# Performance work log

Measured on AMD Instinct MI355X. Metric: run time of the kernel, lower is better.

The kernel has to match this reference:

```python
import jax, jax.numpy as jnp
import numpy as np

T, N, F = 8, 4096, 128
LPF, HPF, H, LP_HID, E = 128, 128, 256, 256, 131072
D = LPF + HPF


def setup_inputs() -> dict:
    key = jax.random.key(0)
    ks = jax.random.split(key, 16)
    s = lambda k, *shape: jax.random.normal(k, shape, dtype=jnp.float32) * 0.05
    feats = jax.random.normal(ks[0], (T, N, F), dtype=jnp.float32)
    # row-stochastic-ish propagation matrices
    p = jax.random.uniform(ks[1], (T, N, N), dtype=jnp.float32)
    p = p / jnp.sum(p, axis=-1, keepdims=True)
    eidx = jax.random.randint(ks[2], (2, E), 0, N, dtype=jnp.int64)
    return {
        "features": feats,
        "p_matrix": p,
        "predict_edge_index": eidx,
        "W_lpf": s(ks[3], F, LPF), "b_lpf": jnp.zeros((LPF,), jnp.float32),
        "W_hpf": s(ks[4], F, HPF), "b_hpf": jnp.zeros((HPF,), jnp.float32),
        "W_ih": s(ks[5], 4 * H, D), "W_hh": s(ks[6], 4 * H, H),
        "b_ih": jnp.zeros((4 * H,), jnp.float32), "b_hh": jnp.zeros((4 * H,), jnp.float32),
        "W1": s(ks[7], 2 * H, LP_HID), "b1": jnp.zeros((LP_HID,), jnp.float32),
        "W2": s(ks[8], LP_HID, 1), "b2": jnp.zeros((1,), jnp.float32),
    }


def reference(features, p_matrix, predict_edge_index, W_lpf, b_lpf, W_hpf, b_hpf,
              W_ih, W_hh, b_ih, b_hh, W1, b1, W2, b2):
    # --- batched low/high-pass graph filters over all T snapshots ---
    xw = jnp.einsum('tnf,fd->tnd', features, W_lpf)          # X @ W_lp
    low = jax.nn.relu(jnp.einsum('tnm,tmd->tnd', p_matrix, xw) + b_lpf)
    px = jnp.einsum('tnm,tmf->tnf', p_matrix, features)      # P @ X
    high = jax.nn.relu(jnp.einsum('tnf,fd->tnd', features - px, W_hpf) + b_hpf)
    x_seq = jnp.concatenate([low, high], axis=-1)            # [T, N, D]

    # --- LSTM over time, nodes as batch (torch gate order i,f,g,o) ---
    def step(carry, x_t):
        h, c = carry
        gates = x_t @ W_ih.T + h @ W_hh.T + (b_ih + b_hh)    # [N, 4H]
        i, f, g, o = jnp.split(gates, 4, axis=-1)
        c = jax.nn.sigmoid(f) * c + jax.nn.sigmoid(i) * jnp.tanh(g)
        h = jax.nn.sigmoid(o) * jnp.tanh(c)
        return (h, c), None

    h0 = jnp.zeros((N, H), x_seq.dtype)
    (h_fin, _), _ = jax.lax.scan(step, (h0, h0), x_seq)      # final timestep hidden

    # --- gather + concat + MLP link predictor ---
    src = h_fin[predict_edge_index[0]]
    dst = h_fin[predict_edge_index[1]]
    comb = jnp.concatenate([src, dst], axis=-1)              # [E, 2H]
    hid = jax.nn.relu(comb @ W1 + b1)
    logits = (hid @ W2 + b2).squeeze(-1)                     # [E]
    return logits
```

## Files before the change

kernel.cpp:

```cpp
#include <hip/hip_runtime.h>
#include <stdint.h>

#define T_ 8
#define N_ 4096
#define E_ 131072

typedef __attribute__((ext_vector_type(4))) float f32x4;
typedef __attribute__((ext_vector_type(8))) short s16x8;
typedef __attribute__((ext_vector_type(4))) short s16x4;

static __device__ __forceinline__ short f2bf(float f) {
    union { float f; unsigned u; } v; v.f = f;
    unsigned r = v.u + 0x7fffu + ((v.u >> 16) & 1u);
    return (short)(r >> 16);
}
static __device__ __forceinline__ float bf2f(short s) {
    union { float f; unsigned u; } v; v.u = ((unsigned)(unsigned short)s) << 16;
    return v.f;
}

static __device__ __forceinline__ void bar_nodrain() {
    asm volatile("s_waitcnt lgkmcnt(0)\n\ts_barrier" ::: "memory");
}

__global__ __launch_bounds__(256) void pack_yt(const float* __restrict__ feat,
                                               short* __restrict__ yt) {
    __shared__ float tile[32][33];
    const int t = blockIdx.z, j0 = blockIdx.y * 32, n0 = blockIdx.x * 32;
    const float* src = feat + (size_t)t * N_ * 128 + j0;
    const int jj = threadIdx.x & 31, i4 = threadIdx.x >> 5;
#pragma unroll
    for (int s = 0; s < 4; s++) {
        int ii = i4 * 4 + s;
        tile[ii][jj] = src[(size_t)(n0 + ii) * 128 + jj];
    }
    __syncthreads();
    const int nn = threadIdx.x & 31, j4 = threadIdx.x >> 5;
#pragma unroll
    for (int s = 0; s < 4; s++) {
        int j2 = j4 * 4 + s;
        yt[(size_t)(t * 128 + j0 + j2) * N_ + n0 + nn] = f2bf(tile[nn][j2]);
    }
}

__global__ __launch_bounds__(512) void pfy_gemm(const float* __restrict__ P,
                                                const short* __restrict__ Yt,
                                                float* __restrict__ Z) {
    __shared__ short As[2][128][72];
    __shared__ short Bs[2][128][72];
    const int t = blockIdx.y;
    const int m0 = blockIdx.x * 128;
    const int tid = threadIdx.x;
    const int lane = tid & 63, wid = tid >> 6;
    const int wm = wid >> 2, wn = wid & 3;
    const int frow = lane & 15, kq = lane >> 4;

    const float* Pt = P + (size_t)t * N_ * N_;
    const short* Bt = Yt + (size_t)t * 128 * N_;

    const int ar = tid >> 2;
    const int ak16 = (tid & 3) * 16;
    const int bj = tid >> 2;
    const int bk16 = (tid & 3) * 16;

    f32x4 acc[4][2];
    f32x4 zf = {0.f, 0.f, 0.f, 0.f};
#pragma unroll
    for (int m = 0; m < 4; m++)
#pragma unroll
        for (int n = 0; n < 2; n++) acc[m][n] = zf;

    f32x4 aA[4], aB[4]; s16x8 bA[2], bB[2];

    const float* Pr = &Pt[(size_t)(m0 + ar) * 4096 + ak16];
    const short* Br = &Bt[(size_t)bj * 4096 + bk16];

#define LOADA(KT) do { const int k0_ = (KT) * 64;                              \
        _Pragma("unroll") for (int i = 0; i < 4; i++)                          \
            aA[i] = *(const f32x4*)&Pr[k0_ + i * 4];                           \
        _Pragma("unroll") for (int i = 0; i < 2; i++)                          \
            bA[i] = *(const s16x8*)&Br[k0_ + i * 8]; } while (0)
#define LOADB(KT) do { const int k0_ = (KT) * 64;                              \
        _Pragma("unroll") for (int i = 0; i < 4; i++)                          \
            aB[i] = *(const f32x4*)&Pr[k0_ + i * 4];                           \
        _Pragma("unroll") for (int i = 0; i < 2; i++)                          \
            bB[i] = *(const s16x8*)&Br[k0_ + i * 8]; } while (0)
#define STOREA(BUF) do {                                                       \
        _Pragma("unroll") for (int i = 0; i < 4; i++) {                        \
            s16x4 c4_;                                                         \
            _Pragma("unroll") for (int j = 0; j < 4; j++) c4_[j] = f2bf(aA[i][j]); \
            *(s16x4*)&As[BUF][ar][ak16 + i * 4] = c4_; }                       \
        _Pragma("unroll") for (int i = 0; i < 2; i++)                          \
            *(s16x8*)&Bs[BUF][bj][bk16 + i * 8] = bA[i]; } while (0)
#define STOREB(BUF) do {                                                       \
        _Pragma("unroll") for (int i = 0; i < 4; i++) {                        \
            s16x4 c4_;                                                         \
            _Pragma("unroll") for (int j = 0; j < 4; j++) c4_[j] = f2bf(aB[i][j]); \
            *(s16x4*)&As[BUF][ar][ak16 + i * 4] = c4_; }                       \
        _Pragma("unroll") for (int i = 0; i < 2; i++)                          \
            *(s16x8*)&Bs[BUF][bj][bk16 + i * 8] = bB[i]; } while (0)

    auto compute_t = [&](int buf) {
#pragma unroll
        for (int ks = 0; ks < 2; ks++) {
            s16x8 af[4], bfr[2];
#pragma unroll
            for (int m = 0; m < 4; m++)
                af[m] = *(const s16x8*)&As[buf][wm * 64 + m * 16 + frow][kq * 8 + ks * 32];
#pragma unroll
            for (int n = 0; n < 2; n++)
                bfr[n] = *(const s16x8*)&Bs[buf][wn * 32 + n * 16 + frow][kq * 8 + ks * 32];
#pragma unroll
            for (int m = 0; m < 4; m++)
#pragma unroll
                for (int n = 0; n < 2; n++)
                    acc[m][n] = __builtin_amdgcn_mfma_f32_16x16x32_bf16(af[m], bfr[n], acc[m][n], 0, 0, 0);
        }
    };

    LOADA(0);
    STOREA(0);
    LOADB(1);
    LOADA(2);
    bar_nodrain();

#pragma unroll 2
    for (int kt = 0; kt < 64; kt++) {
        compute_t(kt & 1);
        if (kt < 63) {
            if ((kt & 1) == 0) {
                STOREB(1);
                if (kt + 3 < 64) LOADB(kt + 3);
            } else {
                STOREA(0);
                if (kt + 3 < 64) LOADA(kt + 3);
            }
            bar_nodrain();
        }
    }
#undef LOADA
#undef LOADB
#undef STOREA
#undef STOREB

    float* Zt = Z + (size_t)t * N_ * 128;
#pragma unroll
    for (int m = 0; m < 4; m++)
#pragma unroll
        for (int n = 0; n < 2; n++)
#pragma unroll
            for (int r = 0; r < 4; r++) {
                int row = m0 + wm * 64 + m * 16 + kq * 4 + r;
                int col = wn * 32 + n * 16 + frow;
                Zt[(size_t)row * 128 + col] = acc[m][n][r];
            }
}

__global__ __launch_bounds__(256) void hp2_gemm(const float* __restrict__ feat,
                                                const float* __restrict__ PX,
                                                const float* __restrict__ Wlp,
                                                const float* __restrict__ Whp,
                                                const float* __restrict__ b_lpf,
                                                const float* __restrict__ b_hpf,
                                                short* __restrict__ xhi,
                                                short* __restrict__ xlo) {
    __shared__ float As[32][68];
    __shared__ float Ws[32][132];
    const int m0 = blockIdx.x * 64;
    const int mode = blockIdx.y;
    const float* W = mode ? Whp : Wlp;
    const float* bp = mode ? b_hpf : b_lpf;
    const int tid = threadIdx.x;
    const int rg = tid & 15, cg2 = tid >> 4;
    float acc[4][8];
#pragma unroll
    for (int r = 0; r < 4; r++)
#pragma unroll
        for (int c = 0; c < 8; c++) acc[r][c] = 0.f;

    for (int k0 = 0; k0 < 128; k0 += 32) {
#pragma unroll
        for (int s = 0; s < 2; s++) {
            int q = tid + s * 256, row = q >> 3, k4 = q & 7;
            f32x4 pv = *(const f32x4*)&PX[(size_t)(m0 + row) * 128 + k0 + k4 * 4];
            f32x4 v;
            if (mode) {
                f32x4 fv = *(const f32x4*)&feat[(size_t)(m0 + row) * 128 + k0 + k4 * 4];
#pragma unroll
                for (int i = 0; i < 4; i++) v[i] = fv[i] - pv[i];
            } else {
                v = pv;
            }
#pragma unroll
            for (int i = 0; i < 4; i++) As[k4 * 4 + i][row] = v[i];
        }
#pragma unroll
        for (int s = 0; s < 4; s++) {
            int q = tid + s * 256, kk = q >> 5, j4 = q & 31;
            *(f32x4*)&Ws[kk][j4 * 4] = *(const f32x4*)&W[(size_t)(k0 + kk) * 128 + j4 * 4];
        }
        __syncthreads();
#pragma unroll
        for (int kk = 0; kk < 32; kk++) {
            f32x4 a  = *(const f32x4*)&As[kk][rg * 4];
            f32x4 w0 = *(const f32x4*)&Ws[kk][cg2 * 8];
            f32x4 w1 = *(const f32x4*)&Ws[kk][cg2 * 8 + 4];
#pragma unroll
            for (int r = 0; r < 4; r++)
#pragma unroll
                for (int c = 0; c < 4; c++) {
                    acc[r][c]     += a[r] * w0[c];
                    acc[r][c + 4] += a[r] * w1[c];
                }
        }
        __syncthreads();
    }
    float bh[8];
#pragma unroll
    for (int c = 0; c < 8; c++) bh[c] = bp[cg2 * 8 + c];
#pragma unroll
    for (int r = 0; r < 4; r++) {
        s16x4 h0, h1, l0, l1;
#pragma unroll
        for (int c = 0; c < 4; c++) {
            float v0 = fmaxf(acc[r][c] + bh[c], 0.f);
            float v1 = fmaxf(acc[r][c + 4] + bh[c + 4], 0.f);
            h0[c] = f2bf(v0); l0[c] = f2bf(v0 - bf2f(h0[c]));
            h1[c] = f2bf(v1); l1[c] = f2bf(v1 - bf2f(h1[c]));
        }
        size_t base = (size_t)(m0 + rg * 4 + r) * 256 + mode * 128 + cg2 * 8;
        *(s16x4*)&xhi[base] = h0;  *(s16x4*)&xhi[base + 4] = h1;
        *(s16x4*)&xlo[base] = l0;  *(s16x4*)&xlo[base + 4] = l1;
    }
}

__global__ __launch_bounds__(256) void pack_all(const float* __restrict__ W1,
                                                const float* __restrict__ W_ih,
                                                const float* __restrict__ W_hh,
                                                const float* __restrict__ b_ih,
                                                const float* __restrict__ b_hh,
                                                short* __restrict__ w1chi,
                                                short* __restrict__ w1clo,
                                                short* __restrict__ wchi,
                                                short* __restrict__ wclo,
                                                float* __restrict__ bsum) {
    __shared__ float tile[32][33];
    const int b = blockIdx.x;
    if (b < 512) {
        int idx = (b * 256 + threadIdx.x) * 4;
        int j = idx >> 9, k = idx & 511;
        int orig = (j & 3) * 256 + (j >> 2);
        const float* src = (k < 256) ? &W_ih[(size_t)orig * 256 + k]
                                     : &W_hh[(size_t)orig * 256 + (k - 256)];
        f32x4 v = *(const f32x4*)src;
        s16x4 hi, lo;
#pragma unroll
        for (int i = 0; i < 4; i++) {
            hi[i] = f2bf(v[i]);
            lo[i] = f2bf(v[i] - bf2f(hi[i]));
        }
        *(s16x4*)&wchi[idx] = hi;
        *(s16x4*)&wclo[idx] = lo;
    } else if (b < 640) {
        const int bb = b - 512;
        const int k0 = (bb & 7) * 32;
        const int j0 = (bb >> 3) * 32;
        const int koff = (j0 >= 256) ? 256 : 0;
        const int joff = (j0 >= 256) ? 256 : 0;
        const int jj = threadIdx.x & 31, k4 = threadIdx.x >> 5;
#pragma unroll
        for (int s = 0; s < 4; s++) {
            int kk = k4 * 4 + s;
            tile[kk][jj] = W1[(size_t)(k0 + kk + koff) * 256 + (j0 + jj - joff)];
        }
        __syncthreads();
        const int kk2 = threadIdx.x & 31, j4 = threadIdx.x >> 5;
#pragma unroll
        for (int s = 0; s < 4; s++) {
            int j2 = j4 * 4 + s;
            float v = tile[kk2][j2];
            short hb = f2bf(v);
            w1chi[(size_t)(j0 + j2) * 256 + k0 + kk2] = hb;
            w1clo[(size_t)(j0 + j2) * 256 + k0 + kk2] = f2bf(v - bf2f(hb));
        }
    } else {
#pragma unroll
        for (int s = 0; s < 4; s++) {
            int j = s * 256 + threadIdx.x;
            int orig = (j & 3) * 256 + (j >> 2);
            bsum[j] = b_ih[orig] + b_hh[orig];
        }
    }
}

__global__ __launch_bounds__(512) void lstm_step(const short* __restrict__ xhi,
                                                 const short* __restrict__ xlo,
                                                 const short* __restrict__ hhi_r,
                                                 const short* __restrict__ hlo_r,
                                                 const short* __restrict__ wchi,
                                                 const short* __restrict__ wclo,
                                                 const float* __restrict__ bsum,
                                                 float* __restrict__ cbuf,
                                                 short* __restrict__ hhi_w,
                                                 short* __restrict__ hlo_w,
                                                 int nkt) {
    __shared__ short Ah[2][128][40], Al[2][128][40];
    __shared__ short Bh[2][128][40], Bl[2][128][40];
    __shared__ float gl[128][132];
    const int m0 = blockIdx.x * 128;
    const int j0 = blockIdx.y * 128;
    const int tid = threadIdx.x;
    const int lane = tid & 63, wid = tid >> 6;
    const int wm = wid >> 2, wn = wid & 3;
    const int frow = lane & 15, kq = lane >> 4;

    const int sr = tid >> 2;
    const int sk8 = (tid & 3) * 8;

    f32x4 acc[4][2];
    f32x4 zf = {0.f, 0.f, 0.f, 0.f};
#pragma unroll
    for (int m = 0; m < 4; m++)
#pragma unroll
        for (int n = 0; n < 2; n++) acc[m][n] = zf;

    s16x8 a_h, a_l, b_h, b_l;

    auto load_t = [&](int kt) {
        const int k0 = kt * 32;
        const short* ah = (k0 < 256) ? xhi : hhi_r;
        const short* al = (k0 < 256) ? xlo : hlo_r;
        const size_t abase = (size_t)(m0 + sr) * 256 + (k0 & 255) + sk8;
        a_h = *(const s16x8*)&ah[abase];
        a_l = *(const s16x8*)&al[abase];
        const size_t bb = (size_t)(j0 + sr) * 512 + k0 + sk8;
        b_h = *(const s16x8*)&wchi[bb];
        b_l = *(const s16x8*)&wclo[bb];
    };
    auto store_t = [&](int buf) {
        *(s16x8*)&Ah[buf][sr][sk8] = a_h;
        *(s16x8*)&Al[buf][sr][sk8] = a_l;
        *(s16x8*)&Bh[buf][sr][sk8] = b_h;
        *(s16x8*)&Bl[buf][sr][sk8] = b_l;
    };
    auto compute_t = [&](int buf) {
        s16x8 afh[4], afl[4], bfh[2], bfl[2];
#pragma unroll
        for (int m = 0; m < 4; m++) {
            afh[m] = *(const s16x8*)&Ah[buf][wm * 64 + m * 16 + frow][kq * 8];
            afl[m] = *(const s16x8*)&Al[buf][wm * 64 + m * 16 + frow][kq * 8];
        }
#pragma unroll
        for (int n = 0; n < 2; n++) {
            bfh[n] = *(const s16x8*)&Bh[buf][wn * 32 + n * 16 + frow][kq * 8];
            bfl[n] = *(const s16x8*)&Bl[buf][wn * 32 + n * 16 + frow][kq * 8];
        }
#pragma unroll
        for (int m = 0; m < 4; m++)
#pragma unroll
            for (int n = 0; n < 2; n++) {
                acc[m][n] = __builtin_amdgcn_mfma_f32_16x16x32_bf16(afh[m], bfh[n], acc[m][n], 0, 0, 0);
                acc[m][n] = __builtin_amdgcn_mfma_f32_16x16x32_bf16(afh[m], bfl[n], acc[m][n], 0, 0, 0);
                acc[m][n] = __builtin_amdgcn_mfma_f32_16x16x32_bf16(afl[m], bfh[n], acc[m][n], 0, 0, 0);
            }
    };

    load_t(0);
    store_t(0);
    bar_nodrain();
#pragma unroll 2
    for (int kt = 0; kt < nkt; kt++) {
        const int cur = kt & 1;
        if (kt < nkt - 1) load_t(kt + 1);
        compute_t(cur);
        bar_nodrain();
        if (kt < nkt - 1) { store_t(cur ^ 1); bar_nodrain(); }
    }

#pragma unroll
    for (int m = 0; m < 4; m++)
#pragma unroll
        for (int n = 0; n < 2; n++)
#pragma unroll
            for (int r = 0; r < 4; r++)
                gl[wm * 64 + m * 16 + kq * 4 + r][wn * 32 + n * 16 + frow] = acc[m][n][r];
    bar_nodrain();

    const int erow = tid >> 2;
    const int ec0 = (tid & 3) * 8;
    const size_t cbase = (size_t)(m0 + erow) * 256 + blockIdx.y * 32 + ec0;
    f32x4 co0 = *(const f32x4*)&cbuf[cbase];
    f32x4 co1 = *(const f32x4*)&cbuf[cbase + 4];
    f32x4 cn0, cn1;
    s16x8 h8, l8;
#pragma unroll
    for (int i = 0; i < 8; i++) {
        f32x4 g4 = *(const f32x4*)&gl[erow][(ec0 + i) * 4];
        f32x4 bs = *(const f32x4*)&bsum[j0 + (ec0 + i) * 4];
        float si = 1.f / (1.f + expf(-(g4[0] + bs[0])));
        float sf = 1.f / (1.f + expf(-(g4[1] + bs[1])));
        float tg = tanhf(g4[2] + bs[2]);
        float so = 1.f / (1.f + expf(-(g4[3] + bs[3])));
        float cold = (i < 4) ? co0[i] : co1[i - 4];
        float cn = sf * cold + si * tg;
        float hv = so * tanhf(cn);
        if (i < 4) cn0[i] = cn; else cn1[i - 4] = cn;
        h8[i] = f2bf(hv);
        l8[i] = f2bf(hv - bf2f(h8[i]));
    }
    *(f32x4*)&cbuf[cbase] = cn0;
    *(f32x4*)&cbuf[cbase + 4] = cn1;
    *(s16x8*)&hhi_w[cbase] = h8;
    *(s16x8*)&hlo_w[cbase] = l8;
}

__global__ __launch_bounds__(512) void uv_gemm(const short* __restrict__ hhi,
                                               const short* __restrict__ hlo,
                                               const short* __restrict__ whi,
                                               const short* __restrict__ wlo,
                                               float* __restrict__ UV) {
    __shared__ short Ah[2][128][40], Al[2][128][40];
    __shared__ short Bh[2][128][40], Bl[2][128][40];
    const int m0 = blockIdx.x * 128;
    const int j0 = blockIdx.y * 128;
    const int tid = threadIdx.x;
    const int lane = tid & 63, wid = tid >> 6;
    const int wm = wid >> 2, wn = wid & 3;
    const int frow = lane & 15, kq = lane >> 4;
    const int sr = tid >> 2;
    const int sk8 = (tid & 3) * 8;

    f32x4 acc[4][2];
    f32x4 zf = {0.f, 0.f, 0.f, 0.f};
#pragma unroll
    for (int m = 0; m < 4; m++)
#pragma unroll
        for (int n = 0; n < 2; n++) acc[m][n] = zf;

    s16x8 a_h, a_l, b_h, b_l;

    auto load_t = [&](int kt) {
        const int k0 = kt * 32;
        const size_t abase = (size_t)(m0 + sr) * 256 + k0 + sk8;
        a_h = *(const s16x8*)&hhi[abase];
        a_l = *(const s16x8*)&hlo[abase];
        const size_t bb = (size_t)(j0 + sr) * 256 + k0 + sk8;
        b_h = *(const s16x8*)&whi[bb];
        b_l = *(const s16x8*)&wlo[bb];
    };
    auto store_t = [&](int buf) {
        *(s16x8*)&Ah[buf][sr][sk8] = a_h;
        *(s16x8*)&Al[buf][sr][sk8] = a_l;
        *(s16x8*)&Bh[buf][sr][sk8] = b_h;
        *(s16x8*)&Bl[buf][sr][sk8] = b_l;
    };
    auto compute_t = [&](int buf) {
        s16x8 afh[4], afl[4], bfh[2], bfl[2];
#pragma unroll
        for (int m = 0; m < 4; m++) {
            afh[m] = *(const s16x8*)&Ah[buf][wm * 64 + m * 16 + frow][kq * 8];
            afl[m] = *(const s16x8*)&Al[buf][wm * 64 + m * 16 + frow][kq * 8];
        }
#pragma unroll
        for (int n = 0; n < 2; n++) {
            bfh[n] = *(const s16x8*)&Bh[buf][wn * 32 + n * 16 + frow][kq * 8];
            bfl[n] = *(const s16x8*)&Bl[buf][wn * 32 + n * 16 + frow][kq * 8];
        }
#pragma unroll
        for (int m = 0; m < 4; m++)
#pragma unroll
            for (int n = 0; n < 2; n++) {
                acc[m][n] = __builtin_amdgcn_mfma_f32_16x16x32_bf16(afh[m], bfh[n], acc[m][n], 0, 0, 0);
                acc[m][n] = __builtin_amdgcn_mfma_f32_16x16x32_bf16(afh[m], bfl[n], acc[m][n], 0, 0, 0);
                acc[m][n] = __builtin_amdgcn_mfma_f32_16x16x32_bf16(afl[m], bfh[n], acc[m][n], 0, 0, 0);
            }
    };

    load_t(0);
    store_t(0);
    bar_nodrain();
#pragma unroll 2
    for (int kt = 0; kt < 8; kt++) {
        const int cur = kt & 1;
        if (kt < 7) load_t(kt + 1);
        compute_t(cur);
        bar_nodrain();
        if (kt < 7) { store_t(cur ^ 1); bar_nodrain(); }
    }

#pragma unroll
    for (int m = 0; m < 4; m++)
#pragma unroll
        for (int n = 0; n < 2; n++)
#pragma unroll
            for (int r = 0; r < 4; r++) {
                int row = m0 + wm * 64 + m * 16 + kq * 4 + r;
                int col = j0 + wn * 32 + n * 16 + frow;
                UV[(size_t)row * 512 + col] = acc[m][n][r];
            }
}

__global__ __launch_bounds__(256) void mlp_edge(const float* __restrict__ UV,
                                                const int* __restrict__ eidx,
                                                const float* __restrict__ b1,
                                                const float* __restrict__ W2,
                                                const float* __restrict__ b2,
                                                float* __restrict__ out) {
    const int e = blockIdx.x * 4 + (threadIdx.x >> 6);
    const int lane = threadIdx.x & 63;
    const int c4 = lane * 4;
    const int src = eidx[e];
    const int dst = eidx[E_ + e];
    f32x4 u = *(const f32x4*)&UV[(size_t)src * 512 + c4];
    f32x4 v = *(const f32x4*)&UV[(size_t)dst * 512 + 256 + c4];
    f32x4 bb = *(const f32x4*)&b1[c4];
    f32x4 ww = *(const f32x4*)&W2[c4];
    float p = 0.f;
#pragma unroll
    for (int i = 0; i < 4; i++)
        p += fmaxf(u[i] + v[i] + bb[i], 0.f) * ww[i];
    p += __shfl_xor(p, 1);
    p += __shfl_xor(p, 2);
    p += __shfl_xor(p, 4);
    p += __shfl_xor(p, 8);
    p += __shfl_xor(p, 16);
    p += __shfl_xor(p, 32);
    if (lane == 0) out[e] = p + b2[0];
}

extern "C" void kernel_launch(void* const* d_in, const int* in_sizes, int n_in,
                              void* d_out, int out_size, void* d_ws, size_t ws_size,
                              hipStream_t stream) {
    (void)in_sizes; (void)n_in; (void)out_size; (void)ws_size;
    const float* feat  = (const float*)d_in[0];
    const float* P     = (const float*)d_in[1];
    const int*   eidx  = (const int*)d_in[2];
    const float* W_lpf = (const float*)d_in[3];
    const float* b_lpf = (const float*)d_in[4];
    const float* W_hpf = (const float*)d_in[5];
    const float* b_hpf = (const float*)d_in[6];
    const float* W_ih  = (const float*)d_in[7];
    const float* W_hh  = (const float*)d_in[8];
    const float* b_ih  = (const float*)d_in[9];
    const float* b_hh  = (const float*)d_in[10];
    const float* W1    = (const float*)d_in[11];
    const float* b1    = (const float*)d_in[12];
    const float* W2    = (const float*)d_in[13];
    const float* b2    = (const float*)d_in[14];
    float* out = (float*)d_out;

    char* ws = (char*)d_ws;
    float* xw    = (float*)ws;   ws += (size_t)T_ * N_ * 128 * 4;
    char*  ytreg = ws;           ws += (size_t)T_ * 256 * N_ * 2;
    char*  Zreg  = ws;           ws += (size_t)T_ * N_ * 256 * 4;
    short* xhi   = (short*)ws;   ws += (size_t)T_ * N_ * 256 * 2;
    short* xlo   = (short*)ws;   ws += (size_t)T_ * N_ * 256 * 2;
    (void)xw;

    short* yt    = (short*)ytreg;
    float* PX    = (float*)Zreg;
    float* cbuf  = (float*)ytreg;
    short* hhi0  = (short*)(ytreg + (size_t)N_ * 256 * 4);
    short* hlo0  = hhi0 + (size_t)N_ * 256;
    short* hhi1  = hlo0 + (size_t)N_ * 256;
    short* hlo1  = hhi1 + (size_t)N_ * 256;
    short* w1chi = (short*)Zreg;
    short* w1clo = w1chi + (size_t)512 * 256;
    short* wchi  = w1clo + (size_t)512 * 256;
    short* wclo  = wchi + (size_t)1024 * 512;
    float* bsum  = (float*)(wclo + (size_t)1024 * 512);
    float* UV    = bsum + 1024;

    pack_yt<<<dim3(N_ / 32, 4, T_), 256, 0, stream>>>(feat, yt);
    pfy_gemm<<<dim3(N_ / 128, T_), 512, 0, stream>>>(P, yt, PX);
    hp2_gemm<<<dim3(T_ * N_ / 64, 2), 256, 0, stream>>>(feat, PX, W_lpf, W_hpf,
                                                        b_lpf, b_hpf, xhi, xlo);

    pack_all<<<dim3(641), 256, 0, stream>>>(W1, W_ih, W_hh, b_ih, b_hh,
                                            w1chi, w1clo, wchi, wclo, bsum);

    hipMemsetAsync(cbuf, 0, (size_t)N_ * 256 * 4, stream);

    for (int t = 0; t < T_; t++) {
        const short* hr_hi = (t & 1) ? hhi1 : hhi0;
        const short* hr_lo = (t & 1) ? hlo1 : hlo0;
        short* hw_hi = (t & 1) ? hhi0 : hhi1;
        short* hw_lo = (t & 1) ? hlo0 : hlo1;
        lstm_step<<<dim3(N_ / 128, 1024 / 128), 512, 0, stream>>>(
            xhi + (size_t)t * N_ * 256, xlo + (size_t)t * N_ * 256,
            hr_hi, hr_lo, wchi, wclo, bsum, cbuf, hw_hi, hw_lo,
            (t == 0) ? 8 : 16);
    }

    uv_gemm<<<dim3(N_ / 128, 512 / 128), 512, 0, stream>>>(hhi0, hlo0, w1chi, w1clo, UV);
    mlp_edge<<<dim3(E_ / 4), 256, 0, stream>>>(UV, eidx, b1, W2, b2, out);
}
```

Before: 395.7 us.

## Move filter projection GEMM to split-bf16 MFMA and drop cell-state memset

Replaces the FP32 FMA projection kernel for the low/high-pass filters with an MFMA kernel. It uses split hi/lo bf16 (three products) and double-buffered shared memory, with weights pre-transposed and packed in pack_all. The first LSTM step now treats the cell state as zero instead of reading a memset buffer, which removes the memset launch. The workspace is relocated so packing can run first. The output stores become scalar shorts, which may reduce write efficiency.

```diff
diff --git a/kernel.cpp b/kernel.cpp
--- a/kernel.cpp
+++ b/kernel.cpp
@@ -156,82 +156,117 @@
             }
 }
 
-__global__ __launch_bounds__(256) void hp2_gemm(const float* __restrict__ feat,
-                                                const float* __restrict__ PX,
-                                                const float* __restrict__ Wlp,
-                                                const float* __restrict__ Whp,
-                                                const float* __restrict__ b_lpf,
-                                                const float* __restrict__ b_hpf,
-                                                short* __restrict__ xhi,
-                                                short* __restrict__ xlo) {
-    __shared__ float As[32][68];
-    __shared__ float Ws[32][132];
-    const int m0 = blockIdx.x * 64;
+__global__ __launch_bounds__(512) void hp2m(const float* __restrict__ feat,
+                                            const float* __restrict__ PX,
+                                            const short* __restrict__ wlpT_hi,
+                                            const short* __restrict__ wlpT_lo,
+                                            const short* __restrict__ whpT_hi,
+                                            const short* __restrict__ whpT_lo,
+                                            const float* __restrict__ b_lpf,
+                                            const float* __restrict__ b_hpf,
+                                            short* __restrict__ xhi,
+                                            short* __restrict__ xlo) {
+    __shared__ short Ah[2][128][40], Al[2][128][40];
+    __shared__ short Bh[2][128][40], Bl[2][128][40];
+    const int m0 = blockIdx.x * 128;
     const int mode = blockIdx.y;
-    const float* W = mode ? Whp : Wlp;
+    const short* wT_hi = mode ? whpT_hi : wlpT_hi;
+    const short* wT_lo = mode ? whpT_lo : wlpT_lo;
     const float* bp = mode ? b_hpf : b_lpf;
     const int tid = threadIdx.x;
-    const int rg = tid & 15, cg2 = tid >> 4;
-    float acc[4][8];
-#pragma unroll
-    for (int r = 0; r < 4; r++)
-#pragma unroll
-        for (int c = 0; c < 8; c++) acc[r][c] = 0.f;
-
-    for (int k0 = 0; k0 < 128; k0 += 32) {
-#pragma unroll
-        for (int s = 0; s < 2; s++) {
-            int q = tid + s * 256, row = q >> 3, k4 = q & 7;
-            f32x4 pv = *(const f32x4*)&PX[(size_t)(m0 + row) * 128 + k0 + k4 * 4];
-            f32x4 v;
-            if (mode) {
-                f32x4 fv = *(const f32x4*)&feat[(size_t)(m0 + row) * 128 + k0 + k4 * 4];
-#pragma unroll
-                for (int i = 0; i < 4; i++) v[i] = fv[i] - pv[i];
-            } else {
-                v = pv;
+    const int lane = tid & 63, wid = tid >> 6;
+    const int wm = wid >> 2, wn = wid & 3;
+    const int frow = lane & 15, kq = lane >> 4;
+    const int sr = tid >> 2;
+    const int sk8 = (tid & 3) * 8;
+
+    f32x4 acc[4][2];
+    f32x4 zf = {0.f, 0.f, 0.f, 0.f};
+#pragma unroll
+    for (int m = 0; m < 4; m++)
+#pragma unroll
+        for (int n = 0; n < 2; n++) acc[m][n] = zf;
+
+    f32x4 v0, v1; s16x8 b_h, b_l;
+
+    auto load_t = [&](int kt) {
+        const int k0 = kt * 32;
+        const size_t abase = (size_t)(m0 + sr) * 128 + k0 + sk8;
+        v0 = *(const f32x4*)&PX[abase];
+        v1 = *(const f32x4*)&PX[abase + 4];
+        if (mode) {
+            f32x4 f0 = *(const f32x4*)&feat[abase];
+            f32x4 f1 = *(const f32x4*)&feat[abase + 4];
+#pragma unroll
+            for (int i = 0; i < 4; i++) { v0[i] = f0[i] - v0[i]; v1[i] = f1[i] - v1[i]; }
+        }
+        const size_t bb = (size_t)sr * 128 + k0 + sk8;
+        b_h = *(const s16x8*)&wT_hi[bb];
+        b_l = *(const s16x8*)&wT_lo[bb];
+    };
+    auto store_t = [&](int buf) {
+        s16x8 hi8, lo8;
+#pragma unroll
+        for (int i = 0; i < 4; i++) {
+            hi8[i] = f2bf(v0[i]);     lo8[i] = f2bf(v0[i] - bf2f(hi8[i]));
+            hi8[i + 4] = f2bf(v1[i]); lo8[i + 4] = f2bf(v1[i] - bf2f(hi8[i + 4]));
+        }
+        *(s16x8*)&Ah[buf][sr][sk8] = hi8;
+        *(s16x8*)&Al[buf][sr][sk8] = lo8;
+        *(s16x8*)&Bh[buf][sr][sk8] = b_h;
+        *(s16x8*)&Bl[buf][sr][sk8] = b_l;
+    };
+    auto compute_t = [&](int buf) {
+        s16x8 afh[4], afl[4], bfh[2], bfl[2];
+#pragma unroll
+        for (int m = 0; m < 4; m++) {
+            afh[m] = *(const s16x8*)&Ah[buf][wm * 64 + m * 16 + frow][kq * 8];
+            afl[m] = *(const s16x8*)&Al[buf][wm * 64 + m * 16 + frow][kq * 8];
+        }
+#pragma unroll
+        for (int n = 0; n < 2; n++) {
+            bfh[n] = *(const s16x8*)&Bh[buf][wn * 32 + n * 16 + frow][kq * 8];
+            bfl[n] = *(const s16x8*)&Bl[buf][wn * 32 + n * 16 + frow][kq * 8];
+        }
+#pragma unroll
+        for (int m = 0; m < 4; m++)
+#pragma unroll
+            for (int n = 0; n < 2; n++) {
+                acc[m][n] = __builtin_amdgcn_mfma_f32_16x16x32_bf16(afh[m], bfh[n], acc[m][n], 0, 0, 0);
+                acc[m][n] = __builtin_amdgcn_mfma_f32_16x16x32_bf16(afh[m], bfl[n], acc[m][n], 0, 0, 0);
+                acc[m][n] = __builtin_amdgcn_mfma_f32_16x16x32_bf16(afl[m], bfh[n], acc[m][n], 0, 0, 0);
             }
-#pragma unroll
-            for (int i = 0; i < 4; i++) As[k4 * 4 + i][row] = v[i];
-        }
-#pragma unroll
-        for (int s = 0; s < 4; s++) {
-            int q = tid + s * 256, kk = q >> 5, j4 = q & 31;
-            *(f32x4*)&Ws[kk][j4 * 4] = *(const f32x4*)&W[(size_t)(k0 + kk) * 128 + j4 * 4];
-        }
-        __syncthreads();
-#pragma unroll
-        for (int kk = 0; kk < 32; kk++) {
-            f32x4 a  = *(const f32x4*)&As[kk][rg * 4];
-            f32x4 w0 = *(const f32x4*)&Ws[kk][cg2 * 8];
-            f32x4 w1 = *(const f32x4*)&Ws[kk][cg2 * 8 + 4];
-#pragma unroll
-            for (int r = 0; r < 4; r++)
-#pragma unroll
-                for (int c = 0; c < 4; c++) {
-                    acc[r][c]     += a[r] * w0[c];
-                    acc[r][c + 4] += a[r] * w1[c];
-                }
-        }
-        __syncthreads();
-    }
-    float bh[8];
-#pragma unroll
-    for (int c = 0; c < 8; c++) bh[c] = bp[cg2 * 8 + c];
-#pragma unroll
-    for (int r = 0; r < 4; r++) {
-        s16x4 h0, h1, l0, l1;
-#pragma unroll
-        for (int c = 0; c < 4; c++) {
-            float v0 = fmaxf(acc[r][c] + bh[c], 0.f);
-            float v1 = fmaxf(acc[r][c + 4] + bh[c + 4], 0.f);
-            h0[c] = f2bf(v0); l0[c] = f2bf(v0 - bf2f(h0[c]));
-            h1[c] = f2bf(v1); l1[c] = f2bf(v1 - bf2f(h1[c]));
-        }
-        size_t base = (size_t)(m0 + rg * 4 + r) * 256 + mode * 128 + cg2 * 8;
-        *(s16x4*)&xhi[base] = h0;  *(s16x4*)&xhi[base + 4] = h1;
-        *(s16x4*)&xlo[base] = l0;  *(s16x4*)&xlo[base + 4] = l1;
-    }
+    };
+
+    load_t(0);
+    store_t(0);
+    bar_nodrain();
+#pragma unroll
+    for (int kt = 0; kt < 4; kt++) {
+        const int cur = kt & 1;
+        if (kt < 3) load_t(kt + 1);
+        compute_t(cur);
+        bar_nodrain();
+        if (kt < 3) { store_t(cur ^ 1); bar_nodrain(); }
+    }
+
+    float bv[2];
+#pragma unroll
+    for (int n = 0; n < 2; n++) bv[n] = bp[wn * 32 + n * 16 + frow];
+#pragma unroll
+    for (int m = 0; m < 4; m++)
+#pragma unroll
+        for (int n = 0; n < 2; n++)
+#pragma unroll
+            for (int r = 0; r < 4; r++) {
+                int row = m0 + wm * 64 + m * 16 + kq * 4 + r;
+                int col = wn * 32 + n * 16 + frow;
+                float val = fmaxf(acc[m][n][r] + bv[n], 0.f);
+                short hb = f2bf(val);
+                size_t o = (size_t)row * 256 + mode * 128 + col;
+                xhi[o] = hb;
+                xlo[o] = f2bf(val - bf2f(hb));
+            }
 }
 
 __global__ __launch_bounds__(256) void pack_all(const float* __restrict__ W1,
@@ -239,11 +274,17 @@
                                                 const float* __restrict__ W_hh,
                                                 const float* __restrict__ b_ih,
                                                 const float* __restrict__ b_hh,
+                                                const float* __restrict__ W_lpf,
+                                                const float* __restrict__ W_hpf,
                                                 short* __restrict__ w1chi,
                                                 short* __restrict__ w1clo,
                                                 short* __restrict__ wchi,
                                                 short* __restrict__ wclo,
-                                                float* __restrict__ bsum) {
+                                                float* __restrict__ bsum,
+                                                short* __restrict__ wlpT_hi,
+                                                short* __restrict__ wlpT_lo,
+                                                short* __restrict__ whpT_hi,
+                                                short* __restrict__ whpT_lo) {
     __shared__ float tile[32][33];
     const int b = blockIdx.x;
     if (b < 512) {
@@ -283,12 +324,37 @@
             w1chi[(size_t)(j0 + j2) * 256 + k0 + kk2] = hb;
             w1clo[(size_t)(j0 + j2) * 256 + k0 + kk2] = f2bf(v - bf2f(hb));
         }
-    } else {
+    } else if (b == 640) {
 #pragma unroll
         for (int s = 0; s < 4; s++) {
             int j = s * 256 + threadIdx.x;
             int orig = (j & 3) * 256 + (j >> 2);
             bsum[j] = b_ih[orig] + b_hh[orig];
+        }
+    } else {
+        const int bb2 = b - 641;
+        const int wsel = bb2 >> 4;
+        const int t16 = bb2 & 15;
+        const int k0 = (t16 & 3) * 32;
+        const int j0 = (t16 >> 2) * 32;
+        const float* Wsrc = wsel ? W_hpf : W_lpf;
+        short* dhi = wsel ? whpT_hi : wlpT_hi;
+        short* dlo = wsel ? whpT_lo : wlpT_lo;
+        const int jj = threadIdx.x & 31, k4 = threadIdx.x >> 5;
+#pragma unroll
+        for (int s = 0; s < 4; s++) {
+            int kk = k4 * 4 + s;
+            tile[kk][jj] = Wsrc[(size_t)(k0 + kk) * 128 + (j0 + jj)];
+        }
+        __syncthreads();
+        const int kk2 = threadIdx.x & 31, j4 = threadIdx.x >> 5;
+#pragma unroll
+        for (int s = 0; s < 4; s++) {
+            int j2 = j4 * 4 + s;
+            float v = tile[kk2][j2];
+            short hb = f2bf(v);
+            dhi[(size_t)(j0 + j2) * 128 + k0 + kk2] = hb;
+            dlo[(size_t)(j0 + j2) * 128 + k0 + kk2] = f2bf(v - bf2f(hb));
         }
     }
 }
@@ -303,7 +369,7 @@
                                                  float* __restrict__ cbuf,
                                                  short* __restrict__ hhi_w,
                                                  short* __restrict__ hlo_w,
-                                                 int nkt) {
+                                                 int nkt, int czero) {
     __shared__ short Ah[2][128][40], Al[2][128][40];
     __shared__ short Bh[2][128][40], Bl[2][128][40];
     __shared__ float gl[128][132];
@@ -389,8 +455,11 @@
     const int erow = tid >> 2;
     const int ec0 = (tid & 3) * 8;
     const size_t cbase = (size_t)(m0 + erow) * 256 + blockIdx.y * 32 + ec0;
-    f32x4 co0 = *(const f32x4*)&cbuf[cbase];
-    f32x4 co1 = *(const f32x4*)&cbuf[cbase + 4];
+    f32x4 co0 = {0.f, 0.f, 0.f, 0.f}, co1 = {0.f, 0.f, 0.f, 0.f};
+    if (!czero) {
+        co0 = *(const f32x4*)&cbuf[cbase];
+        co1 = *(const f32x4*)&cbuf[cbase + 4];
+    }
     f32x4 cn0, cn1;
     s16x8 h8, l8;
 #pragma unroll
@@ -550,12 +619,21 @@
     float* out = (float*)d_out;
 
     char* ws = (char*)d_ws;
-    float* xw    = (float*)ws;   ws += (size_t)T_ * N_ * 128 * 4;
+    char*  pkreg = ws;           ws += (size_t)T_ * N_ * 128 * 4;
     char*  ytreg = ws;           ws += (size_t)T_ * 256 * N_ * 2;
     char*  Zreg  = ws;           ws += (size_t)T_ * N_ * 256 * 4;
     short* xhi   = (short*)ws;   ws += (size_t)T_ * N_ * 256 * 2;
     short* xlo   = (short*)ws;   ws += (size_t)T_ * N_ * 256 * 2;
-    (void)xw;
+
+    short* w1chi = (short*)pkreg;
+    short* w1clo = w1chi + (size_t)512 * 256;
+    short* wchi  = w1clo + (size_t)512 * 256;
+    short* wclo  = wchi + (size_t)1024 * 512;
+    float* bsum  = (float*)(wclo + (size_t)1024 * 512);
+    short* wlpT_hi = (short*)(bsum + 1024);
+    short* wlpT_lo = wlpT_hi + 128 * 128;
+    short* whpT_hi = wlpT_lo + 128 * 128;
+    short* whpT_lo = whpT_hi + 128 * 128;
 
     short* yt    = (short*)ytreg;
     float* PX    = (float*)Zreg;
@@ -564,22 +642,16 @@
     short* hlo0  = hhi0 + (size_t)N_ * 256;
     short* hhi1  = hlo0 + (size_t)N_ * 256;
     short* hlo1  = hhi1 + (size_t)N_ * 256;
-    short* w1chi = (short*)Zreg;
-    short* w1clo = w1chi + (size_t)512 * 256;
-    short* wchi  = w1clo + (size_t)512 * 256;
-    short* wclo  = wchi + (size_t)1024 * 512;
-    float* bsum  = (float*)(wclo + (size_t)1024 * 512);
-    float* UV    = bsum + 1024;
-
+    float* UV    = (float*)Zreg;
+
+    pack_all<<<dim3(673), 256, 0, stream>>>(W1, W_ih, W_hh, b_ih, b_hh, W_lpf, W_hpf,
+                                            w1chi, w1clo, wchi, wclo, bsum,
+                                            wlpT_hi, wlpT_lo, whpT_hi, whpT_lo);
     pack_yt<<<dim3(N_ / 32, 4, T_), 256, 0, stream>>>(feat, yt);
     pfy_gemm<<<dim3(N_ / 128, T_), 512, 0, stream>>>(P, yt, PX);
-    hp2_gemm<<<dim3(T_ * N_ / 64, 2), 256, 0, stream>>>(feat, PX, W_lpf, W_hpf,
-                                                        b_lpf, b_hpf, xhi, xlo);
-
-    pack_all<<<dim3(641), 256, 0, stream>>>(W1, W_ih, W_hh, b_ih, b_hh,
-                                            w1chi, w1clo, wchi, wclo, bsum);
-
-    hipMemsetAsync(cbuf, 0, (size_t)N_ * 256 * 4, stream);
+    hp2m<<<dim3(T_ * N_ / 128, 2), 512, 0, stream>>>(feat, PX, wlpT_hi, wlpT_lo,
+                                                     whpT_hi, whpT_lo, b_lpf, b_hpf,
+                                                     xhi, xlo);
 
     for (int t = 0; t < T_; t++) {
         const short* hr_hi = (t & 1) ? hhi1 : hhi0;
@@ -589,7 +661,7 @@
         lstm_step<<<dim3(N_ / 128, 1024 / 128), 512, 0, stream>>>(
             xhi + (size_t)t * N_ * 256, xlo + (size_t)t * N_ * 256,
             hr_hi, hr_lo, wchi, wclo, bsum, cbuf, hw_hi, hw_lo,
-            (t == 0) ? 8 : 16);
+            (t == 0) ? 8 : 16, (t == 0) ? 1 : 0);
     }
 
     uv_gemm<<<dim3(N_ / 128, 512 / 128), 512, 0, stream>>>(hhi0, hlo0, w1chi, w1clo, UV);
```

Measured after the change: 384.8 us. -2.8%, faster.
